# Kernel optimization log

Measured on AMD Instinct MI355X. Metric: run time of the kernel, lower is better.

Reference implementation:

```python
import jax, jax.numpy as jnp
import numpy as np

N, C, K, G, E = 65536, 256, 128, 32, 2097152
LN_EPS = 1e-5


def setup_inputs() -> dict:
    key = jax.random.key(0)
    ks = jax.random.split(key, 16)
    inp = {
        "x": jax.random.normal(ks[0], (N, C), jnp.float32),
        "evals_batch": jax.random.uniform(ks[1], (G * K,), jnp.float32),
        "evecs": jax.random.normal(ks[2], (N, K), jnp.float32),
        "mass": jax.random.uniform(ks[3], (N,), jnp.float32),
        "row": jax.random.randint(ks[4], (E,), 0, N),
        "col": jax.random.randint(ks[5], (E,), 0, N),
        "vals": jax.random.normal(ks[6], (E,), jnp.float32),
        # learned parameters (torch Linear convention: weight is [out, in])
        "t_params": jnp.full((C,), 0.5, jnp.float32),
        "grad_W": jax.random.normal(ks[7], (C, C), jnp.float32) / np.sqrt(C),
        "grad_b": jnp.zeros((C,), jnp.float32),
        "W1": jax.random.normal(ks[8], (C, 2 * C), jnp.float32) / np.sqrt(2 * C),
        "b1": jnp.zeros((C,), jnp.float32),
        "W2": jax.random.normal(ks[9], (C, C), jnp.float32) / np.sqrt(C),
        "b2": jnp.zeros((C,), jnp.float32),
        "ln_g": jnp.ones((C,), jnp.float32),
        "ln_b": jnp.zeros((C,), jnp.float32),
    }
    return inp


def reference(x, evals_batch, evecs, mass, row, col, vals,
              t_params, grad_W, grad_b, W1, b1, W2, b2, ln_g, ln_b):
    # batch is contiguous with G equal-size graphs of n nodes each
    n = N // G
    t = jnp.abs(t_params)                                   # [C]
    xg = x.reshape(G, n, C)
    eg = evecs.reshape(G, n, K)
    mg = mass.reshape(G, n)
    ev = evals_batch.reshape(G, K)
    # spectral diffusion, batched over graphs
    x_spec = jnp.einsum('gnk,gnc->gkc', eg, xg * mg[..., None])      # [G,K,C]
    decay = jnp.exp(-t[None, None, :] * jnp.clip(ev, 0.0)[..., None])  # [G,K,C]
    diff_out = jnp.einsum('gnk,gkc->gnc', eg, x_spec * decay).reshape(N, C)
    # sparse gradient operator: grad_feat = grad_X_sparse @ x  (COO)
    grad_feat = jax.ops.segment_sum(vals[:, None] * x[col], row, num_segments=N)
    grad_feat = grad_feat @ grad_W.T + grad_b
    # MLP (dropout is identity at eval)
    fused = jnp.concatenate([diff_out, grad_feat], axis=-1)           # [N,2C]
    h = jax.nn.relu(fused @ W1.T + b1)
    fused = h @ W2.T + b2
    # residual + LayerNorm
    y = x + fused
    mu = jnp.mean(y, axis=-1, keepdims=True)
    var = jnp.var(y, axis=-1, keepdims=True)
    return (y - mu) * jax.lax.rsqrt(var + LN_EPS) * ln_g + ln_b
```

## Files before the change

### kernel.cpp

```cpp
#include <hip/hip_runtime.h>

typedef unsigned short u16;
typedef unsigned long long u64;
using short8 = __attribute__((ext_vector_type(8))) short;
using f32x4  = __attribute__((ext_vector_type(4))) float;

constexpr int N_  = 65536;
constexpr int C_  = 256;
constexpr int K_  = 128;
constexpr int G_  = 32;
constexpr int NG_ = 2048;
constexpr int E_  = 2097152;
constexpr int NBIN_ = 2048;
constexpr int CAPB_ = 1280;

__device__ __forceinline__ u16 f2bf(float f) {
  unsigned u = __float_as_uint(f);
  unsigned r = u + 0x7FFF + ((u >> 16) & 1);
  return (u16)(r >> 16);
}
__device__ __forceinline__ float bf2f(u16 h) { return __uint_as_float((unsigned)h << 16); }

__device__ __forceinline__ void gload_lds16(const void* g, void* l) {
  __builtin_amdgcn_global_load_lds((const __attribute__((address_space(1))) void*)g,
                                   (__attribute__((address_space(3))) void*)l, 16, 0, 0);
}

constexpr int PA_SCAT = 128;
constexpr int PA_CVX  = 4096;
constexpr int PA_CVE  = 2048;
constexpr int PA_W1   = 512;
constexpr int PA_W2   = 256;
constexpr int PA_T256 = 16;
constexpr int PA_TOTAL = PA_SCAT + PA_CVX + PA_CVE + PA_W1 + PA_W2 + PA_T256 + 1;

__global__ __launch_bounds__(256) void k_phaseA(
    const int* __restrict__ row, const int* __restrict__ col, const float* __restrict__ vals,
    int* __restrict__ gcnt, u64* __restrict__ epB,
    const float* __restrict__ x, const float* __restrict__ mass,
    u16* __restrict__ xbf, u16* __restrict__ xmT,
    const float* __restrict__ evecs, u16* __restrict__ Ebf, u16* __restrict__ EbfT,
    const float* __restrict__ W1, u16* __restrict__ W1bf,
    const float* __restrict__ W2, u16* __restrict__ W2bf,
    const float* __restrict__ gW, u16* __restrict__ gWT,
    const float* __restrict__ gb, const float* __restrict__ b1, float* __restrict__ bc) {
  __shared__ __align__(16) char smem[3 * NBIN_ * 4];
  float (*tile)[65] = (float(*)[65])smem;
  float* msm = (float*)(smem + 64 * 65 * 4);
  int id = blockIdx.x, tid = threadIdx.x;

  if (id < PA_SCAT) {
    int* hist  = (int*)smem;
    int* lbase = hist + NBIN_;
    int* cur   = lbase + NBIN_;
    #pragma unroll
    for (int j = 0; j < 8; ++j) { hist[tid + j * 256] = 0; cur[tid + j * 256] = 0; }
    __syncthreads();
    int e0 = id * 16384 + tid;
    #pragma unroll 4
    for (int i = 0; i < 64; ++i) {
      int b = row[e0 + i * 256] >> 5;
      atomicAdd(&hist[b], 1);
    }
    __syncthreads();
    #pragma unroll
    for (int j = 0; j < 8; ++j) {
      int b = tid + j * 256;
      int h = hist[b];
      lbase[b] = h ? atomicAdd(&gcnt[b], h) : 0;
    }
    __syncthreads();
    #pragma unroll 4
    for (int i = 0; i < 64; ++i) {
      int e = e0 + i * 256;
      int rr = row[e];
      int b = rr >> 5;
      int rk = atomicAdd(&cur[b], 1);
      int pos = lbase[b] + rk;
      if (pos < CAPB_)
        epB[(size_t)b * CAPB_ + pos] =
            ((u64)(rr & 31) << 32) | ((u64)f2bf(vals[e]) << 16) | (u64)(unsigned)col[e];
    }
    return;
  }
  id -= PA_SCAT;
  if (id < PA_CVX) {
    int r0 = (id >> 2) * 64, c0 = (id & 3) * 64;
    int tr = tid >> 4, tc4 = (tid & 15) * 4;
    #pragma unroll
    for (int p = 0; p < 4; ++p) {
      int r = p * 16 + tr;
      float4 v = *(const float4*)&x[(size_t)(r0 + r) * C_ + c0 + tc4];
      tile[r][tc4 + 0] = v.x; tile[r][tc4 + 1] = v.y; tile[r][tc4 + 2] = v.z; tile[r][tc4 + 3] = v.w;
      ushort4 o = {f2bf(v.x), f2bf(v.y), f2bf(v.z), f2bf(v.w)};
      *(ushort4*)&xbf[(size_t)(r0 + r) * C_ + c0 + tc4] = o;
    }
    if (tid < 64) msm[tid] = mass[r0 + tid];
    __syncthreads();
    int g = r0 >> 11, n0 = r0 & (NG_ - 1);
    #pragma unroll
    for (int p = 0; p < 4; ++p) {
      int cl = p * 16 + tr;
      ushort4 o;
      o.x = f2bf(tile[tc4 + 0][cl] * msm[tc4 + 0]);
      o.y = f2bf(tile[tc4 + 1][cl] * msm[tc4 + 1]);
      o.z = f2bf(tile[tc4 + 2][cl] * msm[tc4 + 2]);
      o.w = f2bf(tile[tc4 + 3][cl] * msm[tc4 + 3]);
      *(ushort4*)&xmT[((size_t)g * C_ + c0 + cl) * NG_ + n0 + tc4] = o;
    }
    return;
  }
  id -= PA_CVX;
  if (id < PA_CVE) {
    int r0 = (id >> 1) * 64, c0 = (id & 1) * 64;
    int tr = tid >> 4, tc4 = (tid & 15) * 4;
    #pragma unroll
    for (int p = 0; p < 4; ++p) {
      int r = p * 16 + tr;
      float4 v = *(const float4*)&evecs[(size_t)(r0 + r) * K_ + c0 + tc4];
      tile[r][tc4 + 0] = v.x; tile[r][tc4 + 1] = v.y; tile[r][tc4 + 2] = v.z; tile[r][tc4 + 3] = v.w;
      ushort4 o = {f2bf(v.x), f2bf(v.y), f2bf(v.z), f2bf(v.w)};
      *(ushort4*)&Ebf[(size_t)(r0 + r) * K_ + c0 + tc4] = o;
    }
    __syncthreads();
    int g = r0 >> 11, n0 = r0 & (NG_ - 1);
    #pragma unroll
    for (int p = 0; p < 4; ++p) {
      int cl = p * 16 + tr;
      ushort4 o = {f2bf(tile[tc4 + 0][cl]), f2bf(tile[tc4 + 1][cl]),
                   f2bf(tile[tc4 + 2][cl]), f2bf(tile[tc4 + 3][cl])};
      *(ushort4*)&EbfT[((size_t)g * K_ + c0 + cl) * NG_ + n0 + tc4] = o;
    }
    return;
  }
  id -= PA_CVE;
  if (id < PA_W1) { int i = id * 256 + tid; W1bf[i] = f2bf(W1[i]); return; }
  id -= PA_W1;
  if (id < PA_W2) { int i = id * 256 + tid; W2bf[i] = f2bf(W2[i]); return; }
  id -= PA_W2;
  if (id < PA_T256) {
    int r0 = (id & 3) * 64, c0 = (id >> 2) * 64;
    int tr = tid >> 4, tc4 = (tid & 15) * 4;
    #pragma unroll
    for (int p = 0; p < 4; ++p) {
      int r = p * 16 + tr;
      float4 v = *(const float4*)&gW[(size_t)(r0 + r) * 256 + c0 + tc4];
      tile[r][tc4 + 0] = v.x; tile[r][tc4 + 1] = v.y; tile[r][tc4 + 2] = v.z; tile[r][tc4 + 3] = v.w;
    }
    __syncthreads();
    #pragma unroll
    for (int p = 0; p < 4; ++p) {
      int cl = p * 16 + tr;
      ushort4 o = {f2bf(tile[tc4 + 0][cl]), f2bf(tile[tc4 + 1][cl]),
                   f2bf(tile[tc4 + 2][cl]), f2bf(tile[tc4 + 3][cl])};
      *(ushort4*)&gWT[(size_t)(c0 + cl) * 256 + r0 + tc4] = o;
    }
    return;
  }
  {
    int c = tid;
    float s = b1[c];
    for (int j = 0; j < 256; ++j) s += W1[(size_t)c * 512 + 256 + j] * gb[j];
    bc[c] = s;
  }
}

__global__ __launch_bounds__(256) void k_gatherC(const u16* __restrict__ xbf, const int* __restrict__ gcnt,
                                                 const u64* __restrict__ epB, u16* __restrict__ gf) {
  __shared__ unsigned eL[CAPB_];
  __shared__ int chist[512], ccur[512];
  __shared__ int roff[513];
  __shared__ int sc[256];
  int b = blockIdx.x, tid = threadIdx.x;
  int wave = tid >> 6, lane = tid & 63;
  int n = gcnt[b]; if (n > CAPB_) n = CAPB_;
  chist[tid] = 0; chist[tid + 256] = 0; ccur[tid] = 0; ccur[tid + 256] = 0;
  __syncthreads();
  const u64* ebase = epB + (size_t)b * CAPB_;
  for (int i = tid; i < n; i += 256) {
    u64 pk = ebase[i];
    int cell = (int)((pk & 0xFFFFu) >> 12) * 32 + (int)((pk >> 32) & 31);
    atomicAdd(&chist[cell], 1);
  }
  __syncthreads();
  int s0 = chist[2 * tid], s1 = chist[2 * tid + 1];
  int s = s0 + s1;
  sc[tid] = s;
  __syncthreads();
  for (int o = 1; o < 256; o <<= 1) {
    int v = (tid >= o) ? sc[tid - o] : 0;
    __syncthreads();
    sc[tid] += v;
    __syncthreads();
  }
  int ex = sc[tid] - s;
  roff[2 * tid] = ex; roff[2 * tid + 1] = ex + s0;
  if (tid == 255) roff[512] = sc[255];
  __syncthreads();
  for (int i = tid; i < n; i += 256) {
    u64 pk = ebase[i];
    int cell = (int)((pk & 0xFFFFu) >> 12) * 32 + (int)((pk >> 32) & 31);
    int rk = atomicAdd(&ccur[cell], 1);
    eL[roff[cell] + rk] = (unsigned)pk;
  }
  __syncthreads();

  const u16* xb = xbf + lane * 4;
  f32x4 acc[8];
  #pragma unroll
  for (int r = 0; r < 8; ++r) acc[r] = {0.f, 0.f, 0.f, 0.f};
  for (int t = 0; t < 16; ++t) {
    #pragma unroll
    for (int rr = 0; rr < 8; ++rr) {
      int cell = t * 32 + wave * 8 + rr;
      int j = roff[cell], en = roff[cell + 1];
      for (; j < en; ++j) {
        unsigned u = eL[j];
        ushort4 xv = *(const ushort4*)(xb + (size_t)(u & 0xFFFFu) * C_);
        float v = bf2f((u16)(u >> 16));
        acc[rr][0] += v * bf2f(xv.x); acc[rr][1] += v * bf2f(xv.y);
        acc[rr][2] += v * bf2f(xv.z); acc[rr][3] += v * bf2f(xv.w);
      }
    }
    __syncthreads();
  }
  int r0 = b * 32 + wave * 8;
  #pragma unroll
  for (int rr = 0; rr < 8; ++rr) {
    ushort4 o = {f2bf(acc[rr][0]), f2bf(acc[rr][1]), f2bf(acc[rr][2]), f2bf(acc[rr][3])};
    *(ushort4*)&gf[(size_t)(r0 + rr) * C_ + lane * 4] = o;
  }
}

constexpr int EPI_BF16  = 0;
constexpr int EPI_DECAY = 3;
constexpr int EPI_TRANS = 4;

template <int BM, int BN, int EPI>
__global__ __launch_bounds__(256) void k_gemm(
    const u16* __restrict__ A, long sAz, int lda,
    const u16* __restrict__ B, long sBz, int ldb,
    int Kd,
    void* __restrict__ outp, long sCz, int ldc,
    const float* __restrict__ tpar, const float* __restrict__ evptr) {
  constexpr int WM = BM / 2, WN = BN / 2;
  constexpr int FM = WM / 16, FN = WN / 16;
  __shared__ __align__(16) u16 Asm[BM * 32];
  __shared__ __align__(16) u16 Bsm[BN * 32];
  int z = blockIdx.z;
  const u16* Ab = A + (long)z * sAz + (long)blockIdx.x * BM * lda;
  const u16* Bb = B + (long)z * sBz + (long)blockIdx.y * BN * ldb;
  int tid = threadIdx.x;
  int wave = tid >> 6, lane = tid & 63;
  int wm = wave >> 1, wn = wave & 1;

  f32x4 acc[FM][FN];
  #pragma unroll
  for (int m = 0; m < FM; ++m)
    #pragma unroll
    for (int n = 0; n < FN; ++n) acc[m][n] = {0.f, 0.f, 0.f, 0.f};

  const u16* aA = Ab + (size_t)(wave * 16 + (lane >> 2)) * lda + (lane & 3) * 8;
  const u16* aB = Bb + (size_t)(wave * 16 + (lane >> 2)) * ldb + (lane & 3) * 8;
  u16* lA = Asm + wave * 512;
  u16* lB = Bsm + wave * 512;
  int arow = wm * WM + (lane & 15);
  int brow = wn * WN + (lane & 15);
  int kof = (lane >> 4) * 8;

  for (int k0 = 0; k0 < Kd; k0 += 32) {
    #pragma unroll
    for (int j = 0; j < BM / 64; ++j) gload_lds16(aA + (size_t)j * 64 * lda + k0, lA + j * 2048);
    #pragma unroll
    for (int j = 0; j < BN / 64; ++j) gload_lds16(aB + (size_t)j * 64 * ldb + k0, lB + j * 2048);
    __syncthreads();
    short8 af[FM], bfr[FN];
    #pragma unroll
    for (int m = 0; m < FM; ++m) af[m] = *(const short8*)(Asm + (arow + m * 16) * 32 + kof);
    #pragma unroll
    for (int n = 0; n < FN; ++n) bfr[n] = *(const short8*)(Bsm + (brow + n * 16) * 32 + kof);
    #pragma unroll
    for (int m = 0; m < FM; ++m)
      #pragma unroll
      for (int n = 0; n < FN; ++n)
        acc[m][n] = __builtin_amdgcn_mfma_f32_16x16x32_bf16(af[m], bfr[n], acc[m][n], 0, 0, 0);
    __syncthreads();
  }

  #pragma unroll
  for (int m = 0; m < FM; ++m) {
    #pragma unroll
    for (int n = 0; n < FN; ++n) {
      int cc = blockIdx.y * BN + wn * WN + n * 16 + (lane & 15);
      int rb = blockIdx.x * BM + wm * WM + m * 16 + ((lane >> 4) << 2);
      if constexpr (EPI == EPI_TRANS) {
        ushort4 o = {f2bf(acc[m][n][0]), f2bf(acc[m][n][1]), f2bf(acc[m][n][2]), f2bf(acc[m][n][3])};
        *(ushort4*)((u16*)outp + (long)z * sCz + (long)cc * ldc + rb) = o;
      } else if constexpr (EPI == EPI_DECAY) {
        float tv = fabsf(tpar[cc]);
        #pragma unroll
        for (int r = 0; r < 4; ++r) {
          float ee = fmaxf(evptr[(size_t)z * K_ + rb + r], 0.f);
          ((u16*)outp)[(long)z * sCz + (long)(rb + r) * ldc + cc] = f2bf(acc[m][n][r] * __expf(-tv * ee));
        }
      } else {
        #pragma unroll
        for (int r = 0; r < 4; ++r)
          ((u16*)outp)[(long)z * sCz + (long)(rb + r) * ldc + cc] = f2bf(acc[m][n][r]);
      }
    }
  }
}

__global__ __launch_bounds__(256) void k_gemm_h2(
    const u16* __restrict__ Eb, const u16* __restrict__ Tt,
    const u16* __restrict__ gf, const u16* __restrict__ Wc,
    const float* __restrict__ bc, u16* __restrict__ h) {
  __shared__ __align__(16) u16 Asm[128 * 32];
  __shared__ __align__(16) u16 Bsm[128 * 32];
  int i0 = blockIdx.x * 128;
  int g = i0 >> 11;
  int tid = threadIdx.x, wave = tid >> 6, lane = tid & 63;
  int wm = wave >> 1, wn = wave & 1;
  f32x4 acc[4][4];
  #pragma unroll
  for (int m = 0; m < 4; ++m)
    #pragma unroll
    for (int n = 0; n < 4; ++n) acc[m][n] = {0.f, 0.f, 0.f, 0.f};
  int srow = wave * 16 + (lane >> 2), scol = (lane & 3) * 8;
  u16* lA = Asm + wave * 512;
  u16* lB = Bsm + wave * 512;
  int arow = wm * 64 + (lane & 15);
  int brow = wn * 64 + (lane & 15);
  int kof = (lane >> 4) * 8;

  {
    const u16* aA = Eb + (size_t)(i0 + srow) * K_ + scol;
    const u16* aB = Tt + (size_t)g * C_ * K_ + (size_t)(blockIdx.y * 128 + srow) * K_ + scol;
    for (int k0 = 0; k0 < 128; k0 += 32) {
      gload_lds16(aA + k0, lA); gload_lds16(aA + (size_t)64 * K_ + k0, lA + 2048);
      gload_lds16(aB + k0, lB); gload_lds16(aB + (size_t)64 * K_ + k0, lB + 2048);
      __syncthreads();
      short8 af[4], bfr[4];
      #pragma unroll
      for (int m = 0; m < 4; ++m) af[m] = *(const short8*)(Asm + (arow + m * 16) * 32 + kof);
      #pragma unroll
      for (int n = 0; n < 4; ++n) bfr[n] = *(const short8*)(Bsm + (brow + n * 16) * 32 + kof);
      #pragma unroll
      for (int m = 0; m < 4; ++m)
        #pragma unroll
        for (int n = 0; n < 4; ++n)
          acc[m][n] = __builtin_amdgcn_mfma_f32_16x16x32_bf16(af[m], bfr[n], acc[m][n], 0, 0, 0);
      __syncthreads();
    }
  }
  {
    const u16* aA = gf + (size_t)(i0 + srow) * C_ + scol;
    const u16* aB = Wc + (size_t)(blockIdx.y * 128 + srow) * C_ + scol;
    for (int k0 = 0; k0 < 256; k0 += 32) {
      gload_lds16(aA + k0, lA); gload_lds16(aA + (size_t)64 * C_ + k0, lA + 2048);
      gload_lds16(aB + k0, lB); gload_lds16(aB + (size_t)64 * C_ + k0, lB + 2048);
      __syncthreads();
      short8 af[4], bfr[4];
      #pragma unroll
      for (int m = 0; m < 4; ++m) af[m] = *(const short8*)(Asm + (arow + m * 16) * 32 + kof);
      #pragma unroll
      for (int n = 0; n < 4; ++n) bfr[n] = *(const short8*)(Bsm + (brow + n * 16) * 32 + kof);
      #pragma unroll
      for (int m = 0; m < 4; ++m)
        #pragma unroll
        for (int n = 0; n < 4; ++n)
          acc[m][n] = __builtin_amdgcn_mfma_f32_16x16x32_bf16(af[m], bfr[n], acc[m][n], 0, 0, 0);
      __syncthreads();
    }
  }
  #pragma unroll
  for (int m = 0; m < 4; ++m) {
    #pragma unroll
    for (int n = 0; n < 4; ++n) {
      int cc = blockIdx.y * 128 + wn * 64 + n * 16 + (lane & 15);
      int rb = i0 + wm * 64 + m * 16 + ((lane >> 4) << 2);
      float bv = bc[cc];
      #pragma unroll
      for (int r = 0; r < 4; ++r)
        h[(size_t)(rb + r) * C_ + cc] = f2bf(fmaxf(acc[m][n][r] + bv, 0.f));
    }
  }
}

__global__ __launch_bounds__(512) void k_out(
    const u16* __restrict__ h, const u16* __restrict__ W2bf, const float* __restrict__ b2,
    const float* __restrict__ x, const float* __restrict__ lng, const float* __restrict__ lnb,
    float* __restrict__ out) {
  __shared__ __align__(16) u16 Asm[128 * 32];
  __shared__ __align__(16) u16 Bsm[256 * 32];
  __shared__ float ps1[128][4], ps2[128][4];
  int i0 = blockIdx.x * 128;
  int tid = threadIdx.x, wave = tid >> 6, lane = tid & 63;
  int wm = wave >> 2, wn = wave & 3;

  f32x4 acc[4][4];
  #pragma unroll
  for (int m = 0; m < 4; ++m)
    #pragma unroll
    for (int n = 0; n < 4; ++n) acc[m][n] = {0.f, 0.f, 0.f, 0.f};

  const u16* aA = h + (size_t)(i0 + (tid >> 2)) * C_ + (tid & 3) * 8;
  const u16* aB = W2bf + (size_t)(tid >> 2) * C_ + (tid & 3) * 8;
  u16* lA = Asm + wave * 512;
  u16* lB = Bsm + wave * 512;
  int arow = wm * 64 + (lane & 15);
  int brow = wn * 64 + (lane & 15);
  int kof = (lane >> 4) * 8;

  for (int k0 = 0; k0 < 256; k0 += 32) {
    gload_lds16(aA + k0, lA);
    gload_lds16(aB + k0, lB);
    gload_lds16(aB + (size_t)128 * C_ + k0, lB + 4096);
    __syncthreads();
    short8 af[4], bfr[4];
    #pragma unroll
    for (int m = 0; m < 4; ++m) af[m] = *(const short8*)(Asm + (arow + m * 16) * 32 + kof);
    #pragma unroll
    for (int n = 0; n < 4; ++n) bfr[n] = *(const short8*)(Bsm + (brow + n * 16) * 32 + kof);
    #pragma unroll
    for (int m = 0; m < 4; ++m)
      #pragma unroll
      for (int n = 0; n < 4; ++n)
        acc[m][n] = __builtin_amdgcn_mfma_f32_16x16x32_bf16(af[m], bfr[n], acc[m][n], 0, 0, 0);
    __syncthreads();
  }

  float bb[4], lg[4], lb[4];
  #pragma unroll
  for (int n = 0; n < 4; ++n) {
    int cc = wn * 64 + n * 16 + (lane & 15);
    bb[n] = b2[cc]; lg[n] = lng[cc]; lb[n] = lnb[cc];
  }
  #pragma unroll
  for (int m = 0; m < 4; ++m) {
    #pragma unroll
    for (int r = 0; r < 4; ++r) {
      int rl = wm * 64 + m * 16 + ((lane >> 4) << 2) + r;
      #pragma unroll
      for (int n = 0; n < 4; ++n) {
        int cc = wn * 64 + n * 16 + (lane & 15);
        acc[m][n][r] += bb[n] + x[(size_t)(i0 + rl) * C_ + cc];
      }
    }
  }
  #pragma unroll
  for (int m = 0; m < 4; ++m) {
    #pragma unroll
    for (int r = 0; r < 4; ++r) {
      float t1 = acc[m][0][r] + acc[m][1][r] + acc[m][2][r] + acc[m][3][r];
      float t2 = acc[m][0][r] * acc[m][0][r] + acc[m][1][r] * acc[m][1][r] +
                 acc[m][2][r] * acc[m][2][r] + acc[m][3][r] * acc[m][3][r];
      #pragma unroll
      for (int msk = 1; msk < 16; msk <<= 1) {
        t1 += __shfl_xor(t1, msk);
        t2 += __shfl_xor(t2, msk);
      }
      if ((lane & 15) == 0) {
        int rl = wm * 64 + m * 16 + ((lane >> 4) << 2) + r;
        ps1[rl][wn] = t1; ps2[rl][wn] = t2;
      }
    }
  }
  __syncthreads();
  #pragma unroll
  for (int m = 0; m < 4; ++m) {
    #pragma unroll
    for (int r = 0; r < 4; ++r) {
      int rl = wm * 64 + m * 16 + ((lane >> 4) << 2) + r;
      float tot1 = ps1[rl][0] + ps1[rl][1] + ps1[rl][2] + ps1[rl][3];
      float tot2 = ps2[rl][0] + ps2[rl][1] + ps2[rl][2] + ps2[rl][3];
      float mu = tot1 * (1.f / 256.f);
      float var = fmaxf(tot2 * (1.f / 256.f) - mu * mu, 0.f);
      float rs = rsqrtf(var + 1e-5f);
      #pragma unroll
      for (int n = 0; n < 4; ++n) {
        int cc = wn * 64 + n * 16 + (lane & 15);
        out[(size_t)(i0 + rl) * C_ + cc] = (acc[m][n][r] - mu) * rs * lg[n] + lb[n];
      }
    }
  }
}

extern "C" void kernel_launch(void* const* d_in, const int* in_sizes, int n_in,
                              void* d_out, int out_size, void* d_ws, size_t ws_size,
                              hipStream_t stream) {
  const float* x        = (const float*)d_in[0];
  const float* ev       = (const float*)d_in[1];
  const float* evecs    = (const float*)d_in[2];
  const float* mass     = (const float*)d_in[3];
  const int*   row      = (const int*)d_in[4];
  const int*   col      = (const int*)d_in[5];
  const float* vals     = (const float*)d_in[6];
  const float* t_params = (const float*)d_in[7];
  const float* gW       = (const float*)d_in[8];
  const float* gb       = (const float*)d_in[9];
  const float* W1       = (const float*)d_in[10];
  const float* b1       = (const float*)d_in[11];
  const float* W2       = (const float*)d_in[12];
  const float* b2       = (const float*)d_in[13];
  const float* lng      = (const float*)d_in[14];
  const float* lnb      = (const float*)d_in[15];
  float* out = (float*)d_out;

  char* p = (char*)d_ws;
  u16* xbf  = (u16*)p; p += (size_t)N_ * C_ * 2;
  u16* xmT  = (u16*)p; p += (size_t)G_ * C_ * NG_ * 2;
  u16* EbfT = (u16*)p; p += (size_t)G_ * K_ * NG_ * 2;
  u16* Ebf  = (u16*)p; p += (size_t)N_ * K_ * 2;
  u16* S    = (u16*)p; p += (size_t)G_ * K_ * C_ * 2;
  u16* Tt   = (u16*)p; p += (size_t)G_ * C_ * K_ * 2;
  u16* h    = (u16*)p; p += (size_t)N_ * C_ * 2;
  u16* W1bf = (u16*)p; p += (size_t)C_ * 512 * 2;
  u16* W2bf = (u16*)p; p += (size_t)C_ * C_ * 2;
  u16* gWT  = (u16*)p; p += (size_t)C_ * C_ * 2;
  u16* Wc   = (u16*)p; p += (size_t)C_ * C_ * 2;
  float* bc = (float*)p; p += (size_t)C_ * 4;
  int* gcnt = (int*)p; p += (size_t)NBIN_ * 4;
  u64* epB  = (u64*)p; p += (size_t)NBIN_ * CAPB_ * 8;
  u16* gf   = xmT;

  hipMemsetAsync(gcnt, 0, (size_t)NBIN_ * 4, stream);

  k_phaseA<<<PA_TOTAL, 256, 0, stream>>>(row, col, vals, gcnt, epB, x, mass, xbf, xmT,
                                         evecs, Ebf, EbfT, W1, W1bf, W2, W2bf,
                                         gW, gWT, gb, b1, bc);

  k_gemm<128, 128, EPI_BF16><<<dim3(2, 2, 1), 256, 0, stream>>>(
      W1bf + 256, 0, 512, gWT, 0, 256, 256, Wc, 0, 256, nullptr, nullptr);
  k_gemm<64, 128, EPI_DECAY><<<dim3(K_ / 64, C_ / 128, G_), 256, 0, stream>>>(
      EbfT, (long)K_ * NG_, NG_, xmT, (long)C_ * NG_, NG_, NG_,
      S, (long)K_ * C_, C_, t_params, ev);
  k_gemm<128, 128, EPI_TRANS><<<dim3(1, 2, G_), 256, 0, stream>>>(
      S, (long)K_ * C_, C_, W1bf, 0, 512, 256,
      Tt, (long)C_ * K_, K_, nullptr, nullptr);

  k_gatherC<<<NBIN_, 256, 0, stream>>>(xbf, gcnt, epB, gf);

  k_gemm_h2<<<dim3(N_ / 128, 2), 256, 0, stream>>>(Ebf, Tt, gf, Wc, bc, h);

  k_out<<<N_ / 128, 512, 0, stream>>>(h, W2bf, b2, x, lng, lnb, out);
}
```

Measured before the change: 388.1 us.

## Restructure sparse gather to row-major cells with batched loads; parallelize bias fold

The gather kernel now sorts edges into cells keyed by destination row first and 32 column chunks of 2048, so each wave processes whole rows in order. Within a row it issues eight independent x-row loads at once before accumulating, which raises memory-level parallelism, and it drops the per-tile block barriers. The single-block bias fold (b1 + W1_grad·gb) is spread over 16 blocks with a shared-memory reduction. This trades the earlier column-tiled locality ordering across waves for more loads in flight per wave.

```diff
diff --git a/kernel.cpp b/kernel.cpp
--- a/kernel.cpp
+++ b/kernel.cpp
@@ -32,7 +32,8 @@
 constexpr int PA_W1   = 512;
 constexpr int PA_W2   = 256;
 constexpr int PA_T256 = 16;
-constexpr int PA_TOTAL = PA_SCAT + PA_CVX + PA_CVE + PA_W1 + PA_W2 + PA_T256 + 1;
+constexpr int PA_BC   = 16;
+constexpr int PA_TOTAL = PA_SCAT + PA_CVX + PA_CVE + PA_W1 + PA_W2 + PA_T256 + PA_BC;
 
 __global__ __launch_bounds__(256) void k_phaseA(
     const int* __restrict__ row, const int* __restrict__ col, const float* __restrict__ vals,
@@ -157,34 +158,48 @@
     }
     return;
   }
+  id -= PA_T256;
   {
-    int c = tid;
-    float s = b1[c];
-    for (int j = 0; j < 256; ++j) s += W1[(size_t)c * 512 + 256 + j] * gb[j];
-    bc[c] = s;
-  }
-}
-
-__global__ __launch_bounds__(256) void k_gatherC(const u16* __restrict__ xbf, const int* __restrict__ gcnt,
+    float* red = (float*)smem;
+    int cl = tid >> 4, js = tid & 15;
+    int c = id * 16 + cl;
+    const float* wrow = &W1[(size_t)c * 512 + 256 + js * 16];
+    float s = 0.f;
+    #pragma unroll
+    for (int jj = 0; jj < 16; ++jj) s += wrow[jj] * gb[js * 16 + jj];
+    red[cl * 17 + js] = s;
+    __syncthreads();
+    if (js == 0) {
+      float tot = b1[c];
+      #pragma unroll
+      for (int q = 0; q < 16; ++q) tot += red[cl * 17 + q];
+      bc[c] = tot;
+    }
+  }
+}
+
+__global__ __launch_bounds__(256) void k_gatherD(const u16* __restrict__ xbf, const int* __restrict__ gcnt,
                                                  const u64* __restrict__ epB, u16* __restrict__ gf) {
   __shared__ unsigned eL[CAPB_];
-  __shared__ int chist[512], ccur[512];
-  __shared__ int roff[513];
+  __shared__ int chist[1024], ccur[1024];
+  __shared__ int roff[1025];
   __shared__ int sc[256];
   int b = blockIdx.x, tid = threadIdx.x;
   int wave = tid >> 6, lane = tid & 63;
   int n = gcnt[b]; if (n > CAPB_) n = CAPB_;
-  chist[tid] = 0; chist[tid + 256] = 0; ccur[tid] = 0; ccur[tid + 256] = 0;
+  #pragma unroll
+  for (int j = 0; j < 4; ++j) { chist[tid + j * 256] = 0; ccur[tid + j * 256] = 0; }
   __syncthreads();
   const u64* ebase = epB + (size_t)b * CAPB_;
   for (int i = tid; i < n; i += 256) {
     u64 pk = ebase[i];
-    int cell = (int)((pk & 0xFFFFu) >> 12) * 32 + (int)((pk >> 32) & 31);
+    int cell = ((int)(pk >> 32) & 31) * 32 + (int)((pk & 0xFFFFu) >> 11);
     atomicAdd(&chist[cell], 1);
   }
   __syncthreads();
-  int s0 = chist[2 * tid], s1 = chist[2 * tid + 1];
-  int s = s0 + s1;
+  int part[4]; int s = 0;
+  #pragma unroll
+  for (int j = 0; j < 4; ++j) { part[j] = chist[tid * 4 + j]; s += part[j]; }
   sc[tid] = s;
   __syncthreads();
   for (int o = 1; o < 256; o <<= 1) {
@@ -194,41 +209,45 @@
     __syncthreads();
   }
   int ex = sc[tid] - s;
-  roff[2 * tid] = ex; roff[2 * tid + 1] = ex + s0;
-  if (tid == 255) roff[512] = sc[255];
+  #pragma unroll
+  for (int j = 0; j < 4; ++j) { roff[tid * 4 + j] = ex; ex += part[j]; }
+  if (tid == 255) roff[1024] = sc[255];
   __syncthreads();
   for (int i = tid; i < n; i += 256) {
     u64 pk = ebase[i];
-    int cell = (int)((pk & 0xFFFFu) >> 12) * 32 + (int)((pk >> 32) & 31);
+    int cell = ((int)(pk >> 32) & 31) * 32 + (int)((pk & 0xFFFFu) >> 11);
     int rk = atomicAdd(&ccur[cell], 1);
     eL[roff[cell] + rk] = (unsigned)pk;
   }
   __syncthreads();
 
   const u16* xb = xbf + lane * 4;
-  f32x4 acc[8];
-  #pragma unroll
-  for (int r = 0; r < 8; ++r) acc[r] = {0.f, 0.f, 0.f, 0.f};
-  for (int t = 0; t < 16; ++t) {
-    #pragma unroll
-    for (int rr = 0; rr < 8; ++rr) {
-      int cell = t * 32 + wave * 8 + rr;
-      int j = roff[cell], en = roff[cell + 1];
-      for (; j < en; ++j) {
-        unsigned u = eL[j];
-        ushort4 xv = *(const ushort4*)(xb + (size_t)(u & 0xFFFFu) * C_);
-        float v = bf2f((u16)(u >> 16));
-        acc[rr][0] += v * bf2f(xv.x); acc[rr][1] += v * bf2f(xv.y);
-        acc[rr][2] += v * bf2f(xv.z); acc[rr][3] += v * bf2f(xv.w);
+  int r0 = b * 32;
+  for (int k = 0; k < 8; ++k) {
+    int r = wave * 8 + k;
+    int j = roff[r * 32], en = roff[r * 32 + 32];
+    float a0 = 0.f, a1 = 0.f, a2 = 0.f, a3 = 0.f;
+    for (; j + 8 <= en; j += 8) {
+      unsigned u[8]; ushort4 xv[8];
+      #pragma unroll
+      for (int q = 0; q < 8; ++q) u[q] = eL[j + q];
+      #pragma unroll
+      for (int q = 0; q < 8; ++q) xv[q] = *(const ushort4*)(xb + (size_t)(u[q] & 0xFFFFu) * C_);
+      #pragma unroll
+      for (int q = 0; q < 8; ++q) {
+        float v = bf2f((u16)(u[q] >> 16));
+        a0 += v * bf2f(xv[q].x); a1 += v * bf2f(xv[q].y);
+        a2 += v * bf2f(xv[q].z); a3 += v * bf2f(xv[q].w);
       }
     }
-    __syncthreads();
-  }
-  int r0 = b * 32 + wave * 8;
-  #pragma unroll
-  for (int rr = 0; rr < 8; ++rr) {
-    ushort4 o = {f2bf(acc[rr][0]), f2bf(acc[rr][1]), f2bf(acc[rr][2]), f2bf(acc[rr][3])};
-    *(ushort4*)&gf[(size_t)(r0 + rr) * C_ + lane * 4] = o;
+    for (; j < en; ++j) {
+      unsigned u = eL[j];
+      ushort4 xv = *(const ushort4*)(xb + (size_t)(u & 0xFFFFu) * C_);
+      float v = bf2f((u16)(u >> 16));
+      a0 += v * bf2f(xv.x); a1 += v * bf2f(xv.y); a2 += v * bf2f(xv.z); a3 += v * bf2f(xv.w);
+    }
+    ushort4 o = {f2bf(a0), f2bf(a1), f2bf(a2), f2bf(a3)};
+    *(ushort4*)&gf[(size_t)(r0 + r) * C_ + lane * 4] = o;
   }
 }
 
@@ -540,7 +559,7 @@
       S, (long)K_ * C_, C_, W1bf, 0, 512, 256,
       Tt, (long)C_ * K_, K_, nullptr, nullptr);
 
-  k_gatherC<<<NBIN_, 256, 0, stream>>>(xbf, gcnt, epB, gf);
+  k_gatherD<<<NBIN_, 256, 0, stream>>>(xbf, gcnt, epB, gf);
 
   k_gemm_h2<<<dim3(N_ / 128, 2), 256, 0, stream>>>(Ebf, Tt, gf, Wc, bc, h);
 
```

New measurement: 394.2 us. Within noise of the previous version (+1.6%).
